# Kernel optimization log

Hardware: AMD Instinct MI355X
Metric: run time of the kernel (lower is better)

Reference implementation:

```python
import jax, jax.numpy as jnp
import numpy as np
from math import sqrt

D_K = 64
HEADS = 16


def setup_inputs() -> dict:
    key = jax.random.key(0)
    k1, k2, k3 = jax.random.split(key, 3)
    B, S, D = 2, 2048, HEADS * D_K
    queries = jax.random.normal(k1, (B, S, D), dtype=jnp.float32)
    keys = jax.random.normal(k2, (B, S, D), dtype=jnp.float32)
    values = jax.random.normal(k3, (B, S, D), dtype=jnp.float32)
    # causal mask: 1 where attention is disallowed (j > i), 0 elsewhere
    mask = jnp.triu(jnp.ones((S, S), dtype=jnp.int32), k=1)[None, None]  # [1,1,S,S]
    return {"queries": queries, "keys": keys, "values": values, "mask": mask}


def reference(queries, keys, values, mask):
    B, S, _ = queries.shape
    # [B, S, H*Dk] -> [B, H, S, Dk]
    def split_heads(x):
        return x.reshape(B, -1, HEADS, D_K).transpose(0, 2, 1, 3)

    q = split_heads(queries)
    k = split_heads(keys)
    v = split_heads(values)
    # scores: [B, H, Sq, Sk]
    attn = jnp.einsum('bhqd,bhkd->bhqk', q, k) / sqrt(D_K)
    attn = attn + mask.astype(attn.dtype) * jnp.asarray(-1e9, attn.dtype)
    w = jax.nn.softmax(attn, axis=-1)
    out = jnp.einsum('bhqk,bhkd->bhqd', w, v)  # [B, H, Sq, Dk]
    return out
```

## Files before the change

kernel.cpp:

```cpp
#include <hip/hip_runtime.h>
#include <hip/hip_bf16.h>

#define S_LEN 2048
#define NH 16
#define DK 64
#define DM 1024
#define QBLK 64
#define KVBLK 64
#define NQT 32
#define KPAD 72

typedef float f32x4 __attribute__((ext_vector_type(4)));
typedef __bf16 bf16x8 __attribute__((ext_vector_type(8)));
typedef __bf16 bf16x4 __attribute__((ext_vector_type(4)));

template <int N>
__device__ __forceinline__ float ror16(float x) {
  return __int_as_float(__builtin_amdgcn_update_dpp(
      0, __float_as_int(x), 0x120 + N , 0xF, 0xF, false));
}
__device__ __forceinline__ float row16_sum(float x) {
  x += ror16<1>(x);
  x += ror16<2>(x);
  x += ror16<4>(x);
  x += ror16<8>(x);
  return x;
}

__device__ __forceinline__ int vswz(int row) { return ((row >> 3) & 3) << 4; }

__device__ __forceinline__ void kv_issue(const float* __restrict__ kp_t,
                                         const float* __restrict__ vp_t,
                                         int tid, int w, int l,
                                         float4 (&kr)[2][2], float (&vr)[16]) {
#pragma unroll
  for (int it = 0; it < 2; ++it) {
    int f = tid + it * 256;
    int row = f >> 3, cb8 = f & 7;
    const float* src = kp_t + (size_t)row * DM + cb8 * 8;
    kr[it][0] = *reinterpret_cast<const float4*>(src);
    kr[it][1] = *reinterpret_cast<const float4*>(src + 4);
  }
#pragma unroll
  for (int it = 0; it < 4; ++it) {
    int kvq = w * 4 + it;
#pragma unroll
    for (int j = 0; j < 4; ++j)
      vr[it * 4 + j] = vp_t[(size_t)(kvq + 16 * j) * DM + l];
  }
}

__device__ __forceinline__ void kv_write(__bf16* __restrict__ Kb, __bf16* __restrict__ Vb,
                                         int tid, int w, int l,
                                         const float4 (&kr)[2][2], const float (&vr)[16]) {
#pragma unroll
  for (int it = 0; it < 2; ++it) {
    int f = tid + it * 256;
    int row = f >> 3, cb8 = f & 7;
    bf16x8 kb;
    kb[0] = (__bf16)kr[it][0].x; kb[1] = (__bf16)kr[it][0].y;
    kb[2] = (__bf16)kr[it][0].z; kb[3] = (__bf16)kr[it][0].w;
    kb[4] = (__bf16)kr[it][1].x; kb[5] = (__bf16)kr[it][1].y;
    kb[6] = (__bf16)kr[it][1].z; kb[7] = (__bf16)kr[it][1].w;
    *reinterpret_cast<bf16x8*>(&Kb[row * KPAD + cb8 * 8]) = kb;
  }
#pragma unroll
  for (int it = 0; it < 4; ++it) {
    int kvq = w * 4 + it;
    bf16x4 vb;
#pragma unroll
    for (int j = 0; j < 4; ++j) vb[j] = (__bf16)vr[it * 4 + j];
    char* p = reinterpret_cast<char*>(Vb) + (((l * KPAD + kvq * 4) * 2) ^ vswz(l));
    *reinterpret_cast<bf16x4*>(p) = vb;
  }
}

__device__ __forceinline__ void mask_diag(f32x4 (&s)[4], int kv0, int q0, int w, int l16, int hi) {
#pragma unroll
  for (int n = 0; n < 4; ++n) {
    const int jg = kv0 + n * 16 + l16;
#pragma unroll
    for (int r = 0; r < 4; ++r) {
      int ig = q0 + w * 16 + hi * 4 + r;
      if (jg > ig) s[n][r] = -1e30f;
    }
  }
}

__device__ __forceinline__ void sm_exp(f32x4 (&s)[4], float (&l_lane)[4]) {
#pragma unroll
  for (int n = 0; n < 4; ++n)
#pragma unroll
    for (int r = 0; r < 4; ++r) {
      float p = __builtin_amdgcn_exp2f(s[n][r]);
      s[n][r] = p;
      l_lane[r] += p;
    }
}

__device__ __forceinline__ void p_store(const f32x4 (&s)[4], __bf16* __restrict__ Pslab,
                                        int l16, int hi) {
#pragma unroll
  for (int r = 0; r < 4; ++r) {
    bf16x4 vb;
#pragma unroll
    for (int n = 0; n < 4; ++n) vb[n] = (__bf16)s[n][r];
    *reinterpret_cast<bf16x4*>(&Pslab[(hi * 4 + r) * KPAD + l16 * 4]) = vb;
  }
}

__device__ __forceinline__ void load_q_frags(const float* __restrict__ qp, int q0,
                                             int w, int l16, int hi, bf16x8 (&aq)[2]) {
  const float* qr = qp + (size_t)(q0 + w * 16 + l16) * DM;
  const float qs = 0.125f * 1.44269504089f;
#pragma unroll
  for (int c = 0; c < 2; ++c) {
    float4 f0 = *reinterpret_cast<const float4*>(qr + c * 32 + hi * 8);
    float4 f1 = *reinterpret_cast<const float4*>(qr + c * 32 + hi * 8 + 4);
    bf16x8 a;
    a[0] = (__bf16)(f0.x * qs); a[1] = (__bf16)(f0.y * qs);
    a[2] = (__bf16)(f0.z * qs); a[3] = (__bf16)(f0.w * qs);
    a[4] = (__bf16)(f1.x * qs); a[5] = (__bf16)(f1.y * qs);
    a[6] = (__bf16)(f1.z * qs); a[7] = (__bf16)(f1.w * qs);
    aq[c] = a;
  }
}

__device__ __forceinline__ void store_out(float* __restrict__ Og, int b, int h, int q0,
                                          int w, int l16, int hi,
                                          const f32x4 (&o_acc)[4], const float (&l_lane)[4]) {
  float inv[4];
#pragma unroll
  for (int r = 0; r < 4; ++r) inv[r] = 1.0f / row16_sum(l_lane[r]);
  float* op = Og + ((size_t)(b * NH + h) * S_LEN + q0 + w * 16) * DK;
#pragma unroll
  for (int n = 0; n < 4; ++n)
#pragma unroll
    for (int r = 0; r < 4; ++r)
      op[(size_t)(hi * 4 + r) * DK + n * 16 + l16] = o_acc[n][r] * inv[r];
}

__global__ __launch_bounds__(256, 2)
void fa_fwd_causal(const float* __restrict__ Qg, const float* __restrict__ Kg,
                   const float* __restrict__ Vg, float* __restrict__ Og) {
  __shared__ __align__(16) __bf16 Kl[2][KVBLK * KPAD];
  __shared__ __align__(16) __bf16 Vt[2][DK * KPAD];
  __shared__ __align__(16) __bf16 Pl[2][QBLK * KPAD];

  const int bid  = blockIdx.x;
  const int xcd  = bid & 7;
  const int s    = bid >> 3;
  const int p_raw = s & 15;
  const int bb   = (s >> 4) & 1;
  const int hh   = (s >> 5) & 1;
  const int pair = hh ? (15 - p_raw) : p_raw;
  const int b    = bb;
  const int h    = xcd + 8 * hh;

  const int qta = pair;
  const int qtb = NQT - 1 - pair;
  const int q0a = qta * QBLK;
  const int q0b = qtb * QBLK;

  const int tid = threadIdx.x;
  const int w   = tid >> 6;
  const int l   = tid & 63;
  const int l16 = l & 15;
  const int hi  = l >> 4;

  const size_t base_in = (size_t)b * S_LEN * DM + (size_t)h * DK;
  const float* qp = Qg + base_in;
  const float* kp = Kg + base_in;
  const float* vp = Vg + base_in;

  bf16x8 aqA[2], aqB[2];
  load_q_frags(qp, q0a, w, l16, hi, aqA);
  load_q_frags(qp, q0b, w, l16, hi, aqB);

  f32x4 oA[4], oB[4];
  float lA[4], lB[4];
#pragma unroll
  for (int n = 0; n < 4; ++n) { oA[n] = (f32x4){0.f,0.f,0.f,0.f}; oB[n] = (f32x4){0.f,0.f,0.f,0.f}; }
#pragma unroll
  for (int r = 0; r < 4; ++r) { lA[r] = 0.f; lB[r] = 0.f; }

  __bf16* PsA = &Pl[0][w * 16 * KPAD];
  __bf16* PsB = &Pl[1][w * 16 * KPAD];

  float4 kr[2][2];
  float  vr[16];
  kv_issue(kp, vp, tid, w, l, kr, vr);

  int cur = 0;
  const int n_tiles = qtb + 1;
  for (int t = 0; t < n_tiles; ++t) {
    const int kv0 = t * KVBLK;
    kv_write(Kl[cur], Vt[cur], tid, w, l, kr, vr);
    if (t + 1 < n_tiles)
      kv_issue(kp + (size_t)(kv0 + KVBLK) * DM, vp + (size_t)(kv0 + KVBLK) * DM,
               tid, w, l, kr, vr);
    __syncthreads();
    const __bf16* Kb = Kl[cur];
    const __bf16* Vb = Vt[cur];

    if (t <= qta) {
      f32x4 sA[4], sB[4];
#pragma unroll
      for (int n = 0; n < 4; ++n) { sA[n] = (f32x4){0.f,0.f,0.f,0.f}; sB[n] = (f32x4){0.f,0.f,0.f,0.f}; }
#pragma unroll
      for (int n = 0; n < 4; ++n)
#pragma unroll
        for (int c = 0; c < 2; ++c) {
          bf16x8 kf = *reinterpret_cast<const bf16x8*>(&Kb[(n * 16 + l16) * KPAD + c * 32 + hi * 8]);
          sB[n] = __builtin_amdgcn_mfma_f32_16x16x32_bf16(aqB[c], kf, sB[n], 0, 0, 0);
          sA[n] = __builtin_amdgcn_mfma_f32_16x16x32_bf16(aqA[c], kf, sA[n], 0, 0, 0);
        }
      if (t == qta) mask_diag(sA, kv0, q0a, w, l16, hi);
      sm_exp(sB, lB);
      sm_exp(sA, lA);
      p_store(sB, PsB, l16, hi);
      p_store(sA, PsA, l16, hi);
#pragma unroll
      for (int c = 0; c < 2; ++c) {
        bf16x8 pfB = *reinterpret_cast<const bf16x8*>(&PsB[l16 * KPAD + c * 32 + hi * 8]);
        bf16x8 pfA = *reinterpret_cast<const bf16x8*>(&PsA[l16 * KPAD + c * 32 + hi * 8]);
#pragma unroll
        for (int n = 0; n < 4; ++n) {
          int row = n * 16 + l16;
          const char* vpb = reinterpret_cast<const char*>(Vb) +
                            (((row * KPAD + c * 32 + hi * 8) * 2) ^ vswz(row));
          bf16x8 vf = *reinterpret_cast<const bf16x8*>(vpb);
          oB[n] = __builtin_amdgcn_mfma_f32_16x16x32_bf16(pfB, vf, oB[n], 0, 0, 0);
          oA[n] = __builtin_amdgcn_mfma_f32_16x16x32_bf16(pfA, vf, oA[n], 0, 0, 0);
        }
      }
    } else {
      f32x4 sB[4];
#pragma unroll
      for (int n = 0; n < 4; ++n) sB[n] = (f32x4){0.f,0.f,0.f,0.f};
#pragma unroll
      for (int n = 0; n < 4; ++n)
#pragma unroll
        for (int c = 0; c < 2; ++c) {
          bf16x8 kf = *reinterpret_cast<const bf16x8*>(&Kb[(n * 16 + l16) * KPAD + c * 32 + hi * 8]);
          sB[n] = __builtin_amdgcn_mfma_f32_16x16x32_bf16(aqB[c], kf, sB[n], 0, 0, 0);
        }
      if (t == qtb) mask_diag(sB, kv0, q0b, w, l16, hi);
      sm_exp(sB, lB);
      p_store(sB, PsB, l16, hi);
#pragma unroll
      for (int c = 0; c < 2; ++c) {
        bf16x8 pfB = *reinterpret_cast<const bf16x8*>(&PsB[l16 * KPAD + c * 32 + hi * 8]);
#pragma unroll
        for (int n = 0; n < 4; ++n) {
          int row = n * 16 + l16;
          const char* vpb = reinterpret_cast<const char*>(Vb) +
                            (((row * KPAD + c * 32 + hi * 8) * 2) ^ vswz(row));
          bf16x8 vf = *reinterpret_cast<const bf16x8*>(vpb);
          oB[n] = __builtin_amdgcn_mfma_f32_16x16x32_bf16(pfB, vf, oB[n], 0, 0, 0);
        }
      }
    }
    cur ^= 1;
  }

  store_out(Og, b, h, q0a, w, l16, hi, oA, lA);
  store_out(Og, b, h, q0b, w, l16, hi, oB, lB);
}

extern "C" void kernel_launch(void* const* d_in, const int* in_sizes, int n_in,
                              void* d_out, int out_size, void* d_ws, size_t ws_size,
                              hipStream_t stream) {
  const float* q = (const float*)d_in[0];
  const float* k = (const float*)d_in[1];
  const float* v = (const float*)d_in[2];
  float* out = (float*)d_out;
  const int blocks = 2 * NH * (NQT / 2);
  hipLaunchKernelGGL(fa_fwd_causal, dim3(blocks), dim3(256), 0, stream, q, k, v, out);
}
```

Before: 48.99 us.

## Compute transposed scores so P feeds PV MFMA from registers, drop LDS P slab

```diff
diff --git a/kernel.cpp b/kernel.cpp
--- a/kernel.cpp
+++ b/kernel.cpp
@@ -12,20 +12,6 @@
 
 typedef float f32x4 __attribute__((ext_vector_type(4)));
 typedef __bf16 bf16x8 __attribute__((ext_vector_type(8)));
-typedef __bf16 bf16x4 __attribute__((ext_vector_type(4)));
-
-template <int N>
-__device__ __forceinline__ float ror16(float x) {
-  return __int_as_float(__builtin_amdgcn_update_dpp(
-      0, __float_as_int(x), 0x120 + N , 0xF, 0xF, false));
-}
-__device__ __forceinline__ float row16_sum(float x) {
-  x += ror16<1>(x);
-  x += ror16<2>(x);
-  x += ror16<4>(x);
-  x += ror16<8>(x);
-  return x;
-}
 
 __device__ __forceinline__ int vswz(int row) { return ((row >> 3) & 3) << 4; }
 
@@ -43,10 +29,9 @@
   }
 #pragma unroll
   for (int it = 0; it < 4; ++it) {
-    int kvq = w * 4 + it;
-#pragma unroll
-    for (int j = 0; j < 4; ++j)
-      vr[it * 4 + j] = vp_t[(size_t)(kvq + 16 * j) * DM + l];
+#pragma unroll
+    for (int r = 0; r < 4; ++r)
+      vr[it * 4 + r] = vp_t[(size_t)(4 * w + 16 * it + r) * DM + l];
   }
 }
 
@@ -65,47 +50,50 @@
     *reinterpret_cast<bf16x8*>(&Kb[row * KPAD + cb8 * 8]) = kb;
   }
 #pragma unroll
-  for (int it = 0; it < 4; ++it) {
-    int kvq = w * 4 + it;
-    bf16x4 vb;
-#pragma unroll
-    for (int j = 0; j < 4; ++j) vb[j] = (__bf16)vr[it * 4 + j];
-    char* p = reinterpret_cast<char*>(Vb) + (((l * KPAD + kvq * 4) * 2) ^ vswz(l));
-    *reinterpret_cast<bf16x4*>(p) = vb;
-  }
-}
-
-__device__ __forceinline__ void mask_diag(f32x4 (&s)[4], int kv0, int q0, int w, int l16, int hi) {
-#pragma unroll
-  for (int n = 0; n < 4; ++n) {
-    const int jg = kv0 + n * 16 + l16;
+  for (int half = 0; half < 2; ++half) {
+    bf16x8 vb;
+#pragma unroll
+    for (int j = 0; j < 8; ++j) vb[j] = (__bf16)vr[half * 8 + j];
+    char* p = reinterpret_cast<char*>(Vb) +
+              (((l * KPAD + half * 32 + w * 8) * 2) ^ vswz(l));
+    *reinterpret_cast<bf16x8*>(p) = vb;
+  }
+}
+
+__device__ __forceinline__ void mask_diagT(f32x4 (&s)[4], int kv0, int q0,
+                                           int w, int l16, int hi) {
+  const int ig = q0 + w * 16 + l16;
+#pragma unroll
+  for (int n = 0; n < 4; ++n)
 #pragma unroll
     for (int r = 0; r < 4; ++r) {
-      int ig = q0 + w * 16 + hi * 4 + r;
+      int jg = kv0 + n * 16 + hi * 4 + r;
       if (jg > ig) s[n][r] = -1e30f;
     }
-  }
-}
-
-__device__ __forceinline__ void sm_exp(f32x4 (&s)[4], float (&l_lane)[4]) {
-#pragma unroll
-  for (int n = 0; n < 4; ++n)
-#pragma unroll
-    for (int r = 0; r < 4; ++r) {
-      float p = __builtin_amdgcn_exp2f(s[n][r]);
-      s[n][r] = p;
-      l_lane[r] += p;
-    }
-}
-
-__device__ __forceinline__ void p_store(const f32x4 (&s)[4], __bf16* __restrict__ Pslab,
-                                        int l16, int hi) {
-#pragma unroll
-  for (int r = 0; r < 4; ++r) {
-    bf16x4 vb;
-#pragma unroll
-    for (int n = 0; n < 4; ++n) vb[n] = (__bf16)s[n][r];
-    *reinterpret_cast<bf16x4*>(&Pslab[(hi * 4 + r) * KPAD + l16 * 4]) = vb;
+}
+
+__device__ __forceinline__ float sm_expT(f32x4 (&s)[4]) {
+  float a0 = 0.f, a1 = 0.f;
+#pragma unroll
+  for (int n = 0; n < 4; ++n) {
+    float p0 = __builtin_amdgcn_exp2f(s[n][0]);
+    float p1 = __builtin_amdgcn_exp2f(s[n][1]);
+    float p2 = __builtin_amdgcn_exp2f(s[n][2]);
+    float p3 = __builtin_amdgcn_exp2f(s[n][3]);
+    s[n][0] = p0; s[n][1] = p1; s[n][2] = p2; s[n][3] = p3;
+    a0 += p0 + p1;
+    a1 += p2 + p3;
+  }
+  return a0 + a1;
+}
+
+__device__ __forceinline__ void packT(const f32x4 (&s)[4], bf16x8 (&pa)[2]) {
+#pragma unroll
+  for (int c = 0; c < 2; ++c) {
+    bf16x8 a;
+#pragma unroll
+    for (int j = 0; j < 8; ++j) a[j] = (__bf16)s[2 * c + (j >> 2)][j & 3];
+    pa[c] = a;
   }
 }
 
@@ -127,11 +115,16 @@
 }
 
 __device__ __forceinline__ void store_out(float* __restrict__ Og, int b, int h, int q0,
-                                          int w, int l16, int hi,
-                                          const f32x4 (&o_acc)[4], const float (&l_lane)[4]) {
+                                          int w, int l, int l16, int hi,
+                                          const f32x4 (&o_acc)[4], float l_chain) {
+  float lf = l_chain;
+  lf += __shfl_xor(lf, 16);
+  lf += __shfl_xor(lf, 32);
+  float invl = 1.0f / lf;
   float inv[4];
 #pragma unroll
-  for (int r = 0; r < 4; ++r) inv[r] = 1.0f / row16_sum(l_lane[r]);
+  for (int r = 0; r < 4; ++r)
+    inv[r] = __shfl(invl, (l & 48) | (hi * 4 + r));
   float* op = Og + ((size_t)(b * NH + h) * S_LEN + q0 + w * 16) * DK;
 #pragma unroll
   for (int n = 0; n < 4; ++n)
@@ -145,7 +138,6 @@
                    const float* __restrict__ Vg, float* __restrict__ Og) {
   __shared__ __align__(16) __bf16 Kl[2][KVBLK * KPAD];
   __shared__ __align__(16) __bf16 Vt[2][DK * KPAD];
-  __shared__ __align__(16) __bf16 Pl[2][QBLK * KPAD];
 
   const int bid  = blockIdx.x;
   const int xcd  = bid & 7;
@@ -178,14 +170,9 @@
   load_q_frags(qp, q0b, w, l16, hi, aqB);
 
   f32x4 oA[4], oB[4];
-  float lA[4], lB[4];
+  float lA = 0.f, lB = 0.f;
 #pragma unroll
   for (int n = 0; n < 4; ++n) { oA[n] = (f32x4){0.f,0.f,0.f,0.f}; oB[n] = (f32x4){0.f,0.f,0.f,0.f}; }
-#pragma unroll
-  for (int r = 0; r < 4; ++r) { lA[r] = 0.f; lB[r] = 0.f; }
-
-  __bf16* PsA = &Pl[0][w * 16 * KPAD];
-  __bf16* PsB = &Pl[1][w * 16 * KPAD];
 
   float4 kr[2][2];
   float  vr[16];
@@ -212,28 +199,26 @@
 #pragma unroll
         for (int c = 0; c < 2; ++c) {
           bf16x8 kf = *reinterpret_cast<const bf16x8*>(&Kb[(n * 16 + l16) * KPAD + c * 32 + hi * 8]);
-          sB[n] = __builtin_amdgcn_mfma_f32_16x16x32_bf16(aqB[c], kf, sB[n], 0, 0, 0);
-          sA[n] = __builtin_amdgcn_mfma_f32_16x16x32_bf16(aqA[c], kf, sA[n], 0, 0, 0);
-        }
-      if (t == qta) mask_diag(sA, kv0, q0a, w, l16, hi);
-      sm_exp(sB, lB);
-      sm_exp(sA, lA);
-      p_store(sB, PsB, l16, hi);
-      p_store(sA, PsA, l16, hi);
-#pragma unroll
-      for (int c = 0; c < 2; ++c) {
-        bf16x8 pfB = *reinterpret_cast<const bf16x8*>(&PsB[l16 * KPAD + c * 32 + hi * 8]);
-        bf16x8 pfA = *reinterpret_cast<const bf16x8*>(&PsA[l16 * KPAD + c * 32 + hi * 8]);
+          sB[n] = __builtin_amdgcn_mfma_f32_16x16x32_bf16(kf, aqB[c], sB[n], 0, 0, 0);
+          sA[n] = __builtin_amdgcn_mfma_f32_16x16x32_bf16(kf, aqA[c], sA[n], 0, 0, 0);
+        }
+      if (t == qta) mask_diagT(sA, kv0, q0a, w, l16, hi);
+      lB += sm_expT(sB);
+      lA += sm_expT(sA);
+      bf16x8 paA[2], paB[2];
+      packT(sB, paB);
+      packT(sA, paA);
+#pragma unroll
+      for (int c = 0; c < 2; ++c)
 #pragma unroll
         for (int n = 0; n < 4; ++n) {
           int row = n * 16 + l16;
           const char* vpb = reinterpret_cast<const char*>(Vb) +
                             (((row * KPAD + c * 32 + hi * 8) * 2) ^ vswz(row));
           bf16x8 vf = *reinterpret_cast<const bf16x8*>(vpb);
-          oB[n] = __builtin_amdgcn_mfma_f32_16x16x32_bf16(pfB, vf, oB[n], 0, 0, 0);
-          oA[n] = __builtin_amdgcn_mfma_f32_16x16x32_bf16(pfA, vf, oA[n], 0, 0, 0);
-        }
-      }
+          oB[n] = __builtin_amdgcn_mfma_f32_16x16x32_bf16(paB[c], vf, oB[n], 0, 0, 0);
+          oA[n] = __builtin_amdgcn_mfma_f32_16x16x32_bf16(paA[c], vf, oA[n], 0, 0, 0);
+        }
     } else {
       f32x4 sB[4];
 #pragma unroll
@@ -243,29 +228,28 @@
 #pragma unroll
         for (int c = 0; c < 2; ++c) {
           bf16x8 kf = *reinterpret_cast<const bf16x8*>(&Kb[(n * 16 + l16) * KPAD + c * 32 + hi * 8]);
-          sB[n] = __builtin_amdgcn_mfma_f32_16x16x32_bf16(aqB[c], kf, sB[n], 0, 0, 0);
-        }
-      if (t == qtb) mask_diag(sB, kv0, q0b, w, l16, hi);
-      sm_exp(sB, lB);
-      p_store(sB, PsB, l16, hi);
-#pragma unroll
-      for (int c = 0; c < 2; ++c) {
-        bf16x8 pfB = *reinterpret_cast<const bf16x8*>(&PsB[l16 * KPAD + c * 32 + hi * 8]);
+          sB[n] = __builtin_amdgcn_mfma_f32_16x16x32_bf16(kf, aqB[c], sB[n], 0, 0, 0);
+        }
+      if (t == qtb) mask_diagT(sB, kv0, q0b, w, l16, hi);
+      lB += sm_expT(sB);
+      bf16x8 paB[2];
+      packT(sB, paB);
+#pragma unroll
+      for (int c = 0; c < 2; ++c)
 #pragma unroll
         for (int n = 0; n < 4; ++n) {
           int row = n * 16 + l16;
           const char* vpb = reinterpret_cast<const char*>(Vb) +
                             (((row * KPAD + c * 32 + hi * 8) * 2) ^ vswz(row));
           bf16x8 vf = *reinterpret_cast<const bf16x8*>(vpb);
-          oB[n] = __builtin_amdgcn_mfma_f32_16x16x32_bf16(pfB, vf, oB[n], 0, 0, 0);
-        }
-      }
+          oB[n] = __builtin_amdgcn_mfma_f32_16x16x32_bf16(paB[c], vf, oB[n], 0, 0, 0);
+        }
     }
     cur ^= 1;
   }
 
-  store_out(Og, b, h, q0a, w, l16, hi, oA, lA);
-  store_out(Og, b, h, q0b, w, l16, hi, oB, lB);
+  store_out(Og, b, h, q0a, w, l, l16, hi, oA, lA);
+  store_out(Og, b, h, q0b, w, l, l16, hi, oB, lB);
 }
 
 extern "C" void kernel_launch(void* const* d_in, const int* in_sizes, int n_in,
```

Result: faster. 43.77 us (-10.7%).
